# Performance work log

Measured on AMD Instinct MI355X. Metric: run time of the kernel, lower is better.

## Reference

```python
import jax, jax.numpy as jnp
import numpy as np
from jax import lax

RGB_H, RGB_W = 288, 256
FOV = 64.0
CAMERA_YAWS = (-60.0, 0.0, 60.0)
CAMERA_X, CAMERA_Z = 1.4, 2.5
MAX_POOL_KS = 7
MAX_DET = 15
NEG_BIG = 100000.0


def _cam_matrices():
    # Intrinsics (same formula as CoordConverter)
    focal = RGB_W / (2.0 * np.tan(FOV * np.pi / 360.0))
    K = np.eye(3, dtype=np.float32)
    K[0, 0] = K[1, 1] = focal
    K[0, 2] = RGB_W / 2.0
    K[1, 2] = RGB_H / 2.0
    # lidar -> world: pure translation by lidar_xyz = [0, 0, camera_z]
    L2W = np.eye(4, dtype=np.float32)
    L2W[2, 3] = CAMERA_Z
    # world -> cam: inverse of (translation cam_xyz, yaw rotation about z)
    W2Cs = []
    for yaw in CAMERA_YAWS:
        r = np.deg2rad(yaw)
        c, s = np.cos(r), np.sin(r)
        M = np.eye(4, dtype=np.float32)
        M[:3, :3] = np.array([[c, -s, 0.0], [s, c, 0.0], [0.0, 0.0, 1.0]], dtype=np.float32)
        M[:3, 3] = np.array([CAMERA_X, 0.0, CAMERA_Z], dtype=np.float32)
        inv = np.eye(4, dtype=np.float32)
        inv[:3, :3] = M[:3, :3].T
        inv[:3, 3] = -M[:3, :3].T @ M[:3, 3]
        W2Cs.append(inv)
    return K, L2W, np.stack(W2Cs)


def setup_inputs() -> dict:
    key = jax.random.key(0)
    k1, k2, k3 = jax.random.split(key, 3)
    N = 2_000_000
    lidar = jax.random.normal(k1, (N, 4), dtype=jnp.float32) * 15.0  # xyz spread ~ tens of meters
    sems = jax.random.uniform(k2, (3, 10, RGB_H, RGB_W), dtype=jnp.float32)
    heatmaps = jax.random.uniform(k3, (2, 640, 640), dtype=jnp.float32)
    K, L2W, W2C = _cam_matrices()
    return {
        "lidar": lidar,
        "sems": sems,
        "heatmaps": heatmaps,
        "K": jnp.asarray(K),
        "lidar_to_world": jnp.asarray(L2W),
        "world_to_cam": jnp.asarray(W2C),
    }


def _project(lidar, K, L2W, W2C):
    # lidar: [N,4] -> integer (u, v, z) camera coords, truncation like torch .long()
    xyz1 = jnp.concatenate([lidar[:, :3], jnp.ones_like(lidar[:, :1])], axis=-1).T  # [4,N]
    world = L2W @ xyz1                                   # [4,N]
    cam = W2C @ world                                    # [4,N]
    cam3 = jnp.stack([cam[1], -cam[2], cam[0]], axis=0)  # [3,N]
    c2 = K @ cam3                                        # [3,N]
    z = 1e-5 + c2[2]
    uvz = jnp.stack([c2[0] / z, c2[1] / z, c2[2]], axis=0).T  # [N,3]
    return uvz.astype(jnp.int32)


def _point_painting(lidar, sems, K, L2W, W2Cs):
    n_cam, sem_c, sem_h, sem_w = sems.shape
    N = lidar.shape[0]
    painted = jnp.zeros((N, sem_c), dtype=lidar.dtype)
    # sequential per-camera overwrite, matching the torch loop semantics
    for i in range(n_cam):
        uvz = _project(lidar, K, L2W, W2Cs[i])
        u, v, z = uvz[:, 0], uvz[:, 1], uvz[:, 2]
        valid = (z >= 0) & (u >= 0) & (u < sem_w) & (v >= 0) & (v < sem_h)
        uc = jnp.clip(u, 0, sem_w - 1)
        vc = jnp.clip(v, 0, sem_h - 1)
        gathered = sems[i][:, vc, uc].T  # [N, sem_c]
        painted = jnp.where(valid[:, None], gathered, painted)
    return painted


def _extract_peak(hm):
    # 7x7 stride-1 max pool with SAME padding, suppress non-peaks, top-k
    mx = lax.reduce_window(hm, -jnp.inf, lax.max,
                           (MAX_POOL_KS, MAX_POOL_KS), (1, 1), "SAME")
    possible = hm - (mx > hm).astype(hm.dtype) * NEG_BIG
    score, loc = lax.top_k(possible.reshape(-1), MAX_DET)
    return score, loc


def reference(lidar, sems, heatmaps, K, lidar_to_world, world_to_cam):
    painted = _point_painting(lidar, sems, K, lidar_to_world, world_to_cam)
    scores, locs = jax.vmap(_extract_peak)(heatmaps)  # [n_cls, 15] each
    return painted, scores, locs
```

## Files before the change

kernel.cpp:

```cpp
#include <hip/hip_runtime.h>
#include <hip/hip_bf16.h>
#include <float.h>
#include <math.h>

#define RGB_H 288
#define RGB_W 256
#define NCH 10
#define NCH_PAD 12
#define HM_N 2
#define HM_S 640
#define MAX_DET_K 15
#define IPT 4
#define PBLK (256 * IPT)

typedef float f4 __attribute__((ext_vector_type(4)));
typedef float f2 __attribute__((ext_vector_type(2)));

#define TW 64
#define TH 16
#define SW (TW + 6)
#define SP 72
#define SH (TH + 6)
#define NTILE_X (HM_S / TW)
#define NTILE_Y (HM_S / TH)
#define TILES_PER_MAP (NTILE_X * NTILE_Y)
#define S1N (TILES_PER_MAP * MAX_DET_K)

#define WS_S1SCORE  0
#define WS_S1IDX    (WS_S1SCORE + HM_N * S1N * 4)
#define WS_PSEMS    ((WS_S1IDX + HM_N * S1N * 4 + 15) & ~15)
#define PSEMS_BYTES ((size_t)3 * RGB_H * RGB_W * NCH_PAD * 4)

__global__ __launch_bounds__(256) void transpose_sems(
    const float* __restrict__ sems, float* __restrict__ ps)
{
    const int t = blockIdx.x * 256 + threadIdx.x;
    const int total = 3 * RGB_H * RGB_W;
    if (t >= total) return;
    const int u = t & (RGB_W - 1);
    const int v = (t >> 8) % RGB_H;
    const int cam = t / (RGB_H * RGB_W);
    float vals[NCH_PAD];
#pragma unroll
    for (int c = 0; c < NCH; ++c)
        vals[c] = sems[(((long long)cam * NCH + c) * RGB_H + v) * RGB_W + u];
    vals[10] = 0.0f; vals[11] = 0.0f;
    f4* dst = (f4*)(ps + (size_t)t * NCH_PAD);
    dst[0] = (f4){vals[0], vals[1], vals[2], vals[3]};
    dst[1] = (f4){vals[4], vals[5], vals[6], vals[7]};
    dst[2] = (f4){vals[8], vals[9], vals[10], vals[11]};
}

__global__ __launch_bounds__(256) void paint_kernel(
    const float* __restrict__ lidar,
    const float* __restrict__ sems,
    const float* __restrict__ psems,
    int use_ps,
    const float* __restrict__ Km,
    const float* __restrict__ L2W,
    const float* __restrict__ W2C,
    float* __restrict__ out,
    int N)
{
    const int tid = threadIdx.x;
    const long long base = (long long)blockIdx.x * PBLK;

    f4 pt[IPT];
#pragma unroll
    for (int k = 0; k < IPT; ++k) {
        const long long p = base + k * 256 + tid;
        if (p < N) pt[k] = __builtin_nontemporal_load(((const f4*)lidar) + p);
        else       pt[k] = (f4){0.f, 0.f, 0.f, 0.f};
    }

    long long gofs[IPT];
#pragma unroll
    for (int k = 0; k < IPT; ++k) {
        const float x = pt[k].x, y = pt[k].y, z = pt[k].z;

        float w[3];
#pragma unroll
        for (int i = 0; i < 3; ++i) {
            float acc = L2W[4*i+0] * x;
            acc = fmaf(L2W[4*i+1], y, acc);
            acc = fmaf(L2W[4*i+2], z, acc);
            acc = fmaf(L2W[4*i+3], 1.0f, acc);
            w[i] = acc;
        }

        int sel = -1, su = 0, sv = 0;
#pragma unroll
        for (int i = 0; i < 3; ++i) {
            const float* W = W2C + 16 * i;
            float cam[3];
#pragma unroll
            for (int r = 0; r < 3; ++r) {
                float acc = W[4*r+0] * w[0];
                acc = fmaf(W[4*r+1], w[1], acc);
                acc = fmaf(W[4*r+2], w[2], acc);
                acc = fmaf(W[4*r+3], 1.0f, acc);
                cam[r] = acc;
            }
            const float c30 = cam[1], c31 = -cam[2], c32 = cam[0];
            float pr[3];
#pragma unroll
            for (int r = 0; r < 3; ++r) {
                float acc = Km[3*r+0] * c30;
                acc = fmaf(Km[3*r+1], c31, acc);
                acc = fmaf(Km[3*r+2], c32, acc);
                pr[r] = acc;
            }
            const float zz = 1e-5f + pr[2];
            const int u  = __float2int_rz(pr[0] / zz);
            const int v  = __float2int_rz(pr[1] / zz);
            const int zi = __float2int_rz(pr[2]);
            const bool valid = (zi >= 0) & (u >= 0) & (u < RGB_W)
                             & (v >= 0) & (v < RGB_H);
            if (valid) { sel = i; su = u; sv = v; }
        }
        gofs[k] = (sel >= 0)
                ? ((long long)sel * RGB_H + sv) * RGB_W + su
                : -1;
        if (base + k * 256 + tid >= N) gofs[k] = -2;
    }

    f4 ga[IPT], gb[IPT]; f2 gc[IPT];
    if (use_ps) {
#pragma unroll
        for (int k = 0; k < IPT; ++k) {
            ga[k] = (f4){0,0,0,0}; gb[k] = (f4){0,0,0,0}; gc[k] = (f2){0,0};
            if (gofs[k] >= 0) {
                const f4* g = (const f4*)(psems + gofs[k] * NCH_PAD);
                ga[k] = g[0]; gb[k] = g[1];
                const f2* g2 = (const f2*)(g + 2);
                gc[k] = g2[0];
            }
        }
    } else {
#pragma unroll
        for (int k = 0; k < IPT; ++k) {
            ga[k] = (f4){0,0,0,0}; gb[k] = (f4){0,0,0,0}; gc[k] = (f2){0,0};
            if (gofs[k] >= 0) {
                const int sel = (int)(gofs[k] / (RGB_H * RGB_W));
                const int pix = (int)(gofs[k] % (RGB_H * RGB_W));
                const float* s = sems + ((long long)sel * NCH) * RGB_H * RGB_W + pix;
                const long long pl = (long long)RGB_H * RGB_W;
                ga[k] = (f4){s[0], s[pl], s[2*pl], s[3*pl]};
                gb[k] = (f4){s[4*pl], s[5*pl], s[6*pl], s[7*pl]};
                gc[k] = (f2){s[8*pl], s[9*pl]};
            }
        }
    }

#pragma unroll
    for (int k = 0; k < IPT; ++k) {
        const long long p = base + k * 256 + tid;
        if (gofs[k] == -2) continue;
        f2* o = (f2*)(out + p * NCH);
        __builtin_nontemporal_store((f2){ga[k].x, ga[k].y}, o + 0);
        __builtin_nontemporal_store((f2){ga[k].z, ga[k].w}, o + 1);
        __builtin_nontemporal_store((f2){gb[k].x, gb[k].y}, o + 2);
        __builtin_nontemporal_store((f2){gb[k].z, gb[k].w}, o + 3);
        __builtin_nontemporal_store(gc[k], o + 4);
    }
}

__global__ __launch_bounds__(256) void peaks15_kernel(
    const float* __restrict__ hm,
    float* __restrict__ s1score,
    int* __restrict__ s1idx)
{
    __shared__ float sA[SH * SP];
    __shared__ float hx[SH * TW];
    __shared__ float lsc[TW * TH];
    __shared__ int   lix[TW * TH];
    __shared__ int   lcnt;

    const int tx = threadIdx.x;
    const int ty = threadIdx.y;
    const int flat = ty * 64 + tx;
    const int gx0 = blockIdx.x * TW;
    const int gy0 = blockIdx.y * TH;
    const int m = blockIdx.z;
    const float* h = hm + (long long)m * HM_S * HM_S;

    if (flat == 0) lcnt = 0;
    __syncthreads();

    for (int yy = ty; yy < SH; yy += 4) {
        const int gv = gy0 + yy - 3;
        const bool vok = (gv >= 0) & (gv < HM_S);
        for (int xx = tx; xx < SW; xx += 64) {
            const int gu = gx0 + xx - 3;
            float val = -INFINITY;
            if (vok & (gu >= 0) & (gu < HM_S)) val = h[gv * HM_S + gu];
            sA[yy * SP + xx] = val;
        }
    }
    __syncthreads();

    for (int yy = ty; yy < SH; yy += 4) {
        const float* r = sA + yy * SP + tx;
        float mx = r[0];
#pragma unroll
        for (int k = 1; k < 7; ++k) mx = fmaxf(mx, r[k]);
        hx[yy * TW + tx] = mx;
    }
    __syncthreads();

    for (int ry = ty; ry < TH; ry += 4) {
        const float val = sA[(ry + 3) * SP + tx + 3];
        float mx = hx[ry * TW + tx];
#pragma unroll
        for (int k = 1; k < 7; ++k) mx = fmaxf(mx, hx[(ry + k) * TW + tx]);
        if (!(mx > val)) {
            int pos = atomicAdd(&lcnt, 1);
            lsc[pos] = val;
            lix[pos] = (gy0 + ry) * HM_S + (gx0 + tx);
        }
    }
    __syncthreads();

    if (flat < 64) {
        const int n = lcnt;
        const int tile = blockIdx.y * NTILE_X + blockIdx.x;
        const int slot0 = (m * TILES_PER_MAP + tile) * MAX_DET_K;
        for (int t = 0; t < MAX_DET_K; ++t) {
            float bs = -INFINITY; int bi = 0x7fffffff; int bp = -1;
            for (int j = flat; j < n; j += 64) {
                const float s = lsc[j]; const int id = lix[j];
                if (s > bs || (s == bs && id < bi)) { bs = s; bi = id; bp = j; }
            }
#pragma unroll
            for (int off = 32; off > 0; off >>= 1) {
                const float os = __shfl_down(bs, off);
                const int   oi = __shfl_down(bi, off);
                const int   op = __shfl_down(bp, off);
                if (os > bs || (os == bs && oi < bi)) { bs = os; bi = oi; bp = op; }
            }
            bs = __shfl(bs, 0); bi = __shfl(bi, 0); bp = __shfl(bp, 0);
            if (flat == 0) {
                s1score[slot0 + t] = bs;
                s1idx[slot0 + t]   = bi;
            }
            if (flat == 0 && bp >= 0) lsc[bp] = -INFINITY;
        }
    }
}

__global__ __launch_bounds__(1024) void merge_kernel(
    const float* __restrict__ s1score,
    const int* __restrict__ s1idx,
    float* __restrict__ out_scores,
    float* __restrict__ out_locs)
{
    const int m = blockIdx.x;
    const int tid = threadIdx.x;
    const int lane = tid & 63;
    const int wv = tid >> 6;

    __shared__ float ls[S1N];
    __shared__ int   li[S1N];
    __shared__ float ws[16];
    __shared__ int   wi[16];
    __shared__ int   wp[16];

    for (int j = tid; j < S1N; j += 1024) {
        ls[j] = s1score[m * S1N + j];
        li[j] = s1idx[m * S1N + j];
    }
    __syncthreads();

    for (int t = 0; t < MAX_DET_K; ++t) {
        float bs = -INFINITY; int bi = 0x7fffffff; int bp = -1;
        for (int j = tid; j < S1N; j += 1024) {
            const float s = ls[j]; const int id = li[j];
            if (s > bs || (s == bs && id < bi)) { bs = s; bi = id; bp = j; }
        }
#pragma unroll
        for (int off = 32; off > 0; off >>= 1) {
            const float os = __shfl_down(bs, off);
            const int   oi = __shfl_down(bi, off);
            const int   op = __shfl_down(bp, off);
            if (os > bs || (os == bs && oi < bi)) { bs = os; bi = oi; bp = op; }
        }
        if (lane == 0) { ws[wv] = bs; wi[wv] = bi; wp[wv] = bp; }
        __syncthreads();
        if (tid < 64) {
            bs = (tid < 16) ? ws[tid] : -INFINITY;
            bi = (tid < 16) ? wi[tid] : 0x7fffffff;
            bp = (tid < 16) ? wp[tid] : -1;
#pragma unroll
            for (int off = 8; off > 0; off >>= 1) {
                const float os = __shfl_down(bs, off);
                const int   oi = __shfl_down(bi, off);
                const int   op = __shfl_down(bp, off);
                if (os > bs || (os == bs && oi < bi)) { bs = os; bi = oi; bp = op; }
            }
            if (tid == 0) {
                out_scores[m * MAX_DET_K + t] = bs;
                out_locs[m * MAX_DET_K + t]   = (float)bi;
                if (bp >= 0) ls[bp] = -INFINITY;
            }
        }
        __syncthreads();
    }
}

extern "C" void kernel_launch(void* const* d_in, const int* in_sizes, int n_in,
                              void* d_out, int out_size, void* d_ws, size_t ws_size,
                              hipStream_t stream)
{
    const float* lidar = (const float*)d_in[0];
    const float* sems  = (const float*)d_in[1];
    const float* hm    = (const float*)d_in[2];
    const float* Km    = (const float*)d_in[3];
    const float* L2W   = (const float*)d_in[4];
    const float* W2C   = (const float*)d_in[5];
    float* out = (float*)d_out;
    const int N = in_sizes[0] / 4;

    char* ws = (char*)d_ws;
    float* s1score = (float*)(ws + WS_S1SCORE);
    int*   s1idx   = (int*)(ws + WS_S1IDX);
    float* psems   = (float*)(ws + WS_PSEMS);
    const int use_ps = (ws_size >= (size_t)WS_PSEMS + PSEMS_BYTES) ? 1 : 0;

    if (use_ps) {
        const int tp_total = 3 * RGB_H * RGB_W;
        transpose_sems<<<(tp_total + 255) / 256, 256, 0, stream>>>(sems, psems);
    }

    paint_kernel<<<(N + PBLK - 1) / PBLK, 256, 0, stream>>>(
        lidar, sems, psems, use_ps, Km, L2W, W2C, out, N);

    dim3 pb(64, 4, 1), pg(NTILE_X, NTILE_Y, HM_N);
    peaks15_kernel<<<pg, pb, 0, stream>>>(hm, s1score, s1idx);

    float* out_scores = out + (long long)N * NCH;
    float* out_locs   = out_scores + HM_N * MAX_DET_K;
    merge_kernel<<<HM_N, 1024, 0, stream>>>(s1score, s1idx, out_scores, out_locs);
}
```

Before: 190.2 us.

## Merge four launches into two by co-scheduling peak extraction with painting

Folds the sems transpose and per-tile peak extraction into one prep kernel that splits work by block index. The merge-top-k step moves into the paint kernel as two leading blocks that hold candidates in registers (24 per thread, 256 threads) rather than using a 1024-thread shared-memory block. The aim is to cut two kernel launches and their serial gaps, and to let the small peak/merge work overlap the large paint pass. The cost is heavier register use in the merge path, and the prep blocks carry the peak kernel's shared memory even when they only transpose, which may lower occupancy.

```diff
diff --git a/kernel.cpp b/kernel.cpp
--- a/kernel.cpp
+++ b/kernel.cpp
@@ -25,33 +25,124 @@
 #define NTILE_Y (HM_S / TH)
 #define TILES_PER_MAP (NTILE_X * NTILE_Y)
 #define S1N (TILES_PER_MAP * MAX_DET_K)
+#define RPT 24
+
+#define TP_TOTAL (3 * RGB_H * RGB_W)
+#define TP_BLOCKS ((TP_TOTAL + 255) / 256)
+#define PEAK_BLOCKS (TILES_PER_MAP * HM_N)
 
 #define WS_S1SCORE  0
 #define WS_S1IDX    (WS_S1SCORE + HM_N * S1N * 4)
 #define WS_PSEMS    ((WS_S1IDX + HM_N * S1N * 4 + 15) & ~15)
 #define PSEMS_BYTES ((size_t)3 * RGB_H * RGB_W * NCH_PAD * 4)
 
-__global__ __launch_bounds__(256) void transpose_sems(
-    const float* __restrict__ sems, float* __restrict__ ps)
+__global__ __launch_bounds__(256) void prep_kernel(
+    const float* __restrict__ sems,
+    const float* __restrict__ hm,
+    float* __restrict__ ps,
+    float* __restrict__ s1score,
+    int* __restrict__ s1idx,
+    int use_ps)
 {
-    const int t = blockIdx.x * 256 + threadIdx.x;
-    const int total = 3 * RGB_H * RGB_W;
-    if (t >= total) return;
-    const int u = t & (RGB_W - 1);
-    const int v = (t >> 8) % RGB_H;
-    const int cam = t / (RGB_H * RGB_W);
-    float vals[NCH_PAD];
-#pragma unroll
-    for (int c = 0; c < NCH; ++c)
-        vals[c] = sems[(((long long)cam * NCH + c) * RGB_H + v) * RGB_W + u];
-    vals[10] = 0.0f; vals[11] = 0.0f;
-    f4* dst = (f4*)(ps + (size_t)t * NCH_PAD);
-    dst[0] = (f4){vals[0], vals[1], vals[2], vals[3]};
-    dst[1] = (f4){vals[4], vals[5], vals[6], vals[7]};
-    dst[2] = (f4){vals[8], vals[9], vals[10], vals[11]};
+    const int bid = blockIdx.x;
+    const int tid = threadIdx.x;
+
+    __shared__ float sA[SH * SP];
+    __shared__ float hx[SH * TW];
+    __shared__ float lsc[TW * TH];
+    __shared__ int   lix[TW * TH];
+    __shared__ int   lcnt;
+
+    if (bid >= PEAK_BLOCKS) {
+        const int t = (bid - PEAK_BLOCKS) * 256 + tid;
+        if (t >= TP_TOTAL) return;
+        const int u = t & (RGB_W - 1);
+        const int v = (t >> 8) % RGB_H;
+        const int cam = t / (RGB_H * RGB_W);
+        float vals[NCH_PAD];
+#pragma unroll
+        for (int c = 0; c < NCH; ++c)
+            vals[c] = sems[(((long long)cam * NCH + c) * RGB_H + v) * RGB_W + u];
+        vals[10] = 0.0f; vals[11] = 0.0f;
+        f4* dst = (f4*)(ps + (size_t)t * NCH_PAD);
+        dst[0] = (f4){vals[0], vals[1], vals[2], vals[3]};
+        dst[1] = (f4){vals[4], vals[5], vals[6], vals[7]};
+        dst[2] = (f4){vals[8], vals[9], vals[10], vals[11]};
+        return;
+    }
+
+    const int m  = bid / TILES_PER_MAP;
+    const int tt = bid % TILES_PER_MAP;
+    const int gx0 = (tt % NTILE_X) * TW;
+    const int gy0 = (tt / NTILE_X) * TH;
+    const int tx = tid & 63;
+    const int ty = tid >> 6;
+    const float* h = hm + (long long)m * HM_S * HM_S;
+
+    if (tid == 0) lcnt = 0;
+    __syncthreads();
+
+    for (int yy = ty; yy < SH; yy += 4) {
+        const int gv = gy0 + yy - 3;
+        const bool vok = (gv >= 0) & (gv < HM_S);
+        for (int xx = tx; xx < SW; xx += 64) {
+            const int gu = gx0 + xx - 3;
+            float val = -INFINITY;
+            if (vok & (gu >= 0) & (gu < HM_S)) val = h[gv * HM_S + gu];
+            sA[yy * SP + xx] = val;
+        }
+    }
+    __syncthreads();
+
+    for (int yy = ty; yy < SH; yy += 4) {
+        const float* r = sA + yy * SP + tx;
+        float mx = r[0];
+#pragma unroll
+        for (int k = 1; k < 7; ++k) mx = fmaxf(mx, r[k]);
+        hx[yy * TW + tx] = mx;
+    }
+    __syncthreads();
+
+    for (int ry = ty; ry < TH; ry += 4) {
+        const float val = sA[(ry + 3) * SP + tx + 3];
+        float mx = hx[ry * TW + tx];
+#pragma unroll
+        for (int k = 1; k < 7; ++k) mx = fmaxf(mx, hx[(ry + k) * TW + tx]);
+        if (!(mx > val)) {
+            int pos = atomicAdd(&lcnt, 1);
+            lsc[pos] = val;
+            lix[pos] = (gy0 + ry) * HM_S + (gx0 + tx);
+        }
+    }
+    __syncthreads();
+
+    if (tid < 64) {
+        const int n = lcnt;
+        const int slot0 = (m * TILES_PER_MAP + tt) * MAX_DET_K;
+        for (int t = 0; t < MAX_DET_K; ++t) {
+            float bs = -INFINITY; int bi = 0x7fffffff; int bp = -1;
+            for (int j = tid; j < n; j += 64) {
+                const float s = lsc[j]; const int id = lix[j];
+                if (s > bs || (s == bs && id < bi)) { bs = s; bi = id; bp = j; }
+            }
+#pragma unroll
+            for (int off = 32; off > 0; off >>= 1) {
+                const float os = __shfl_down(bs, off);
+                const int   oi = __shfl_down(bi, off);
+                const int   op = __shfl_down(bp, off);
+                if (os > bs || (os == bs && oi < bi)) { bs = os; bi = oi; bp = op; }
+            }
+            bs = __shfl(bs, 0); bi = __shfl(bi, 0); bp = __shfl(bp, 0);
+            if (tid == 0) {
+                s1score[slot0 + t] = bs;
+                s1idx[slot0 + t]   = bi;
+                if (bp >= 0) lsc[bp] = -INFINITY;
+            }
+        }
+    }
 }
 
-__global__ __launch_bounds__(256) void paint_kernel(
+__global__ __launch_bounds__(256) void main_kernel(
     const float* __restrict__ lidar,
     const float* __restrict__ sems,
     const float* __restrict__ psems,
@@ -60,10 +151,70 @@
     const float* __restrict__ L2W,
     const float* __restrict__ W2C,
     float* __restrict__ out,
-    int N)
+    int N,
+    const float* __restrict__ s1score,
+    const int* __restrict__ s1idx,
+    float* __restrict__ out_scores,
+    float* __restrict__ out_locs)
 {
     const int tid = threadIdx.x;
-    const long long base = (long long)blockIdx.x * PBLK;
+
+    if (blockIdx.x < HM_N) {
+        const int m = blockIdx.x;
+        const int lane = tid & 63;
+        const int wv = tid >> 6;
+
+        float es[RPT]; int ei[RPT];
+#pragma unroll
+        for (int e = 0; e < RPT; ++e) {
+            const int j = e * 256 + tid;
+            if (j < S1N) { es[e] = s1score[m * S1N + j]; ei[e] = s1idx[m * S1N + j]; }
+            else         { es[e] = -INFINITY;            ei[e] = 0x7fffffff; }
+        }
+
+        __shared__ float bss[4];
+        __shared__ int   bis[4];
+        __shared__ int   bps[4];
+        __shared__ int   fbp;
+
+        for (int t = 0; t < MAX_DET_K; ++t) {
+            float bs = -INFINITY; int bi = 0x7fffffff; int bp = -1;
+#pragma unroll
+            for (int e = 0; e < RPT; ++e) {
+                if (es[e] > bs || (es[e] == bs && ei[e] < bi)) {
+                    bs = es[e]; bi = ei[e]; bp = e * 256 + tid;
+                }
+            }
+#pragma unroll
+            for (int off = 32; off > 0; off >>= 1) {
+                const float os = __shfl_down(bs, off);
+                const int   oi = __shfl_down(bi, off);
+                const int   op = __shfl_down(bp, off);
+                if (os > bs || (os == bs && oi < bi)) { bs = os; bi = oi; bp = op; }
+            }
+            if (lane == 0) { bss[wv] = bs; bis[wv] = bi; bps[wv] = bp; }
+            __syncthreads();
+            if (tid == 0) {
+                float s = bss[0]; int i0 = bis[0]; int p = bps[0];
+#pragma unroll
+                for (int w = 1; w < 4; ++w) {
+                    if (bss[w] > s || (bss[w] == s && bis[w] < i0)) {
+                        s = bss[w]; i0 = bis[w]; p = bps[w];
+                    }
+                }
+                out_scores[m * MAX_DET_K + t] = s;
+                out_locs[m * MAX_DET_K + t]   = (float)i0;
+                fbp = p;
+            }
+            __syncthreads();
+            const int wbp = fbp;
+            if (wbp >= 0 && (wbp & 255) == tid) es[wbp >> 8] = -INFINITY;
+            __syncthreads();
+        }
+        return;
+    }
+
+    const long long base = (long long)(blockIdx.x - HM_N) * PBLK;
 
     f4 pt[IPT];
 #pragma unroll
@@ -162,148 +313,6 @@
         __builtin_nontemporal_store((f2){gb[k].x, gb[k].y}, o + 2);
         __builtin_nontemporal_store((f2){gb[k].z, gb[k].w}, o + 3);
         __builtin_nontemporal_store(gc[k], o + 4);
-    }
-}
-
-__global__ __launch_bounds__(256) void peaks15_kernel(
-    const float* __restrict__ hm,
-    float* __restrict__ s1score,
-    int* __restrict__ s1idx)
-{
-    __shared__ float sA[SH * SP];
-    __shared__ float hx[SH * TW];
-    __shared__ float lsc[TW * TH];
-    __shared__ int   lix[TW * TH];
-    __shared__ int   lcnt;
-
-    const int tx = threadIdx.x;
-    const int ty = threadIdx.y;
-    const int flat = ty * 64 + tx;
-    const int gx0 = blockIdx.x * TW;
-    const int gy0 = blockIdx.y * TH;
-    const int m = blockIdx.z;
-    const float* h = hm + (long long)m * HM_S * HM_S;
-
-    if (flat == 0) lcnt = 0;
-    __syncthreads();
-
-    for (int yy = ty; yy < SH; yy += 4) {
-        const int gv = gy0 + yy - 3;
-        const bool vok = (gv >= 0) & (gv < HM_S);
-        for (int xx = tx; xx < SW; xx += 64) {
-            const int gu = gx0 + xx - 3;
-            float val = -INFINITY;
-            if (vok & (gu >= 0) & (gu < HM_S)) val = h[gv * HM_S + gu];
-            sA[yy * SP + xx] = val;
-        }
-    }
-    __syncthreads();
-
-    for (int yy = ty; yy < SH; yy += 4) {
-        const float* r = sA + yy * SP + tx;
-        float mx = r[0];
-#pragma unroll
-        for (int k = 1; k < 7; ++k) mx = fmaxf(mx, r[k]);
-        hx[yy * TW + tx] = mx;
-    }
-    __syncthreads();
-
-    for (int ry = ty; ry < TH; ry += 4) {
-        const float val = sA[(ry + 3) * SP + tx + 3];
-        float mx = hx[ry * TW + tx];
-#pragma unroll
-        for (int k = 1; k < 7; ++k) mx = fmaxf(mx, hx[(ry + k) * TW + tx]);
-        if (!(mx > val)) {
-            int pos = atomicAdd(&lcnt, 1);
-            lsc[pos] = val;
-            lix[pos] = (gy0 + ry) * HM_S + (gx0 + tx);
-        }
-    }
-    __syncthreads();
-
-    if (flat < 64) {
-        const int n = lcnt;
-        const int tile = blockIdx.y * NTILE_X + blockIdx.x;
-        const int slot0 = (m * TILES_PER_MAP + tile) * MAX_DET_K;
-        for (int t = 0; t < MAX_DET_K; ++t) {
-            float bs = -INFINITY; int bi = 0x7fffffff; int bp = -1;
-            for (int j = flat; j < n; j += 64) {
-                const float s = lsc[j]; const int id = lix[j];
-                if (s > bs || (s == bs && id < bi)) { bs = s; bi = id; bp = j; }
-            }
-#pragma unroll
-            for (int off = 32; off > 0; off >>= 1) {
-                const float os = __shfl_down(bs, off);
-                const int   oi = __shfl_down(bi, off);
-                const int   op = __shfl_down(bp, off);
-                if (os > bs || (os == bs && oi < bi)) { bs = os; bi = oi; bp = op; }
-            }
-            bs = __shfl(bs, 0); bi = __shfl(bi, 0); bp = __shfl(bp, 0);
-            if (flat == 0) {
-                s1score[slot0 + t] = bs;
-                s1idx[slot0 + t]   = bi;
-            }
-            if (flat == 0 && bp >= 0) lsc[bp] = -INFINITY;
-        }
-    }
-}
-
-__global__ __launch_bounds__(1024) void merge_kernel(
-    const float* __restrict__ s1score,
-    const int* __restrict__ s1idx,
-    float* __restrict__ out_scores,
-    float* __restrict__ out_locs)
-{
-    const int m = blockIdx.x;
-    const int tid = threadIdx.x;
-    const int lane = tid & 63;
-    const int wv = tid >> 6;
-
-    __shared__ float ls[S1N];
-    __shared__ int   li[S1N];
-    __shared__ float ws[16];
-    __shared__ int   wi[16];
-    __shared__ int   wp[16];
-
-    for (int j = tid; j < S1N; j += 1024) {
-        ls[j] = s1score[m * S1N + j];
-        li[j] = s1idx[m * S1N + j];
-    }
-    __syncthreads();
-
-    for (int t = 0; t < MAX_DET_K; ++t) {
-        float bs = -INFINITY; int bi = 0x7fffffff; int bp = -1;
-        for (int j = tid; j < S1N; j += 1024) {
-            const float s = ls[j]; const int id = li[j];
-            if (s > bs || (s == bs && id < bi)) { bs = s; bi = id; bp = j; }
-        }
-#pragma unroll
-        for (int off = 32; off > 0; off >>= 1) {
-            const float os = __shfl_down(bs, off);
-            const int   oi = __shfl_down(bi, off);
-            const int   op = __shfl_down(bp, off);
-            if (os > bs || (os == bs && oi < bi)) { bs = os; bi = oi; bp = op; }
-        }
-        if (lane == 0) { ws[wv] = bs; wi[wv] = bi; wp[wv] = bp; }
-        __syncthreads();
-        if (tid < 64) {
-            bs = (tid < 16) ? ws[tid] : -INFINITY;
-            bi = (tid < 16) ? wi[tid] : 0x7fffffff;
-            bp = (tid < 16) ? wp[tid] : -1;
-#pragma unroll
-            for (int off = 8; off > 0; off >>= 1) {
-                const float os = __shfl_down(bs, off);
-                const int   oi = __shfl_down(bi, off);
-                const int   op = __shfl_down(bp, off);
-                if (os > bs || (os == bs && oi < bi)) { bs = os; bi = oi; bp = op; }
-            }
-            if (tid == 0) {
-                out_scores[m * MAX_DET_K + t] = bs;
-                out_locs[m * MAX_DET_K + t]   = (float)bi;
-                if (bp >= 0) ls[bp] = -INFINITY;
-            }
-        }
-        __syncthreads();
     }
 }
 
@@ -326,18 +335,13 @@
     float* psems   = (float*)(ws + WS_PSEMS);
     const int use_ps = (ws_size >= (size_t)WS_PSEMS + PSEMS_BYTES) ? 1 : 0;
 
-    if (use_ps) {
-        const int tp_total = 3 * RGB_H * RGB_W;
-        transpose_sems<<<(tp_total + 255) / 256, 256, 0, stream>>>(sems, psems);
-    }
-
-    paint_kernel<<<(N + PBLK - 1) / PBLK, 256, 0, stream>>>(
-        lidar, sems, psems, use_ps, Km, L2W, W2C, out, N);
-
-    dim3 pb(64, 4, 1), pg(NTILE_X, NTILE_Y, HM_N);
-    peaks15_kernel<<<pg, pb, 0, stream>>>(hm, s1score, s1idx);
+    const int k1_blocks = PEAK_BLOCKS + (use_ps ? TP_BLOCKS : 0);
+    prep_kernel<<<k1_blocks, 256, 0, stream>>>(sems, hm, psems, s1score, s1idx, use_ps);
 
     float* out_scores = out + (long long)N * NCH;
     float* out_locs   = out_scores + HM_N * MAX_DET_K;
-    merge_kernel<<<HM_N, 1024, 0, stream>>>(s1score, s1idx, out_scores, out_locs);
+    const int paint_blocks = (int)((N + PBLK - 1) / PBLK);
+    main_kernel<<<HM_N + paint_blocks, 256, 0, stream>>>(
+        lidar, sems, psems, use_ps, Km, L2W, W2C, out, N,
+        s1score, s1idx, out_scores, out_locs);
 }
```

New measurement: 158.0 us. 16.9% less time.
